# Kernel optimization log

Measured on AMD Instinct MI355X. Metric: run time of the kernel, lower is better.

## Reference

```python
import jax, jax.numpy as jnp
import numpy as np

B, L, D = 16, 2048, 320          # batch, frames, stacked feature dim (80 mel * 4 reduction)
CODEBOOK_SIZE, CODEBOOK_DIM = 8192, 16


def setup_inputs() -> dict:
    key = jax.random.key(0)
    k1, k2, k3 = jax.random.split(key, 3)
    masked_target_values = jax.random.normal(k1, (B, L, D), dtype=jnp.float32)
    # xavier_uniform_ for shape (D, codebook_dim): bound = sqrt(6/(fan_in+fan_out))
    bound = np.sqrt(6.0 / (D + CODEBOOK_DIM)).astype(np.float32)
    project_mat = jax.random.uniform(k2, (D, CODEBOOK_DIM), dtype=jnp.float32,
                                     minval=-bound, maxval=bound)
    cb = jax.random.normal(k3, (CODEBOOK_SIZE, CODEBOOK_DIM), dtype=jnp.float32)
    codebook_norm = cb / jnp.maximum(jnp.linalg.norm(cb, axis=-1, keepdims=True), 1e-12)
    return {"masked_target_values": masked_target_values,
            "project_mat": project_mat,
            "codebook_norm": codebook_norm}


def reference(masked_target_values, project_mat, codebook_norm):
    # project: (B, L, D) @ (D, K) -> (B, L, K)
    targets = jnp.einsum('bld,dk->blk', masked_target_values, project_mat)
    # L2 normalize along last dim (torch F.normalize with eps=1e-12)
    targets_norm = targets / jnp.maximum(
        jnp.linalg.norm(targets, axis=-1, keepdims=True), 1e-12)
    x2 = jnp.sum(targets_norm * targets_norm, axis=-1, keepdims=True)      # (B, L, 1)
    c2 = jnp.sum(codebook_norm * codebook_norm, axis=-1)                   # (C,)
    xc = jnp.einsum('blk,ck->blc', targets_norm, codebook_norm)            # (B, L, C)
    d2 = jnp.maximum(x2 + c2[None, None, :] - 2.0 * xc, 0.0)
    vector_distances = jnp.sqrt(d2)
    labels = jnp.argmin(vector_distances, axis=-1)                         # (B, L) int
    return labels
```

## Files before the change

kernel.cpp:

```cpp
#include <hip/hip_runtime.h>
#include <cfloat>

#define TOKENS 32768
#define DIM    320
#define NCODE  8192
#define PROW   20
#define APAD   40
#define NTILE  64
#define CERT_UNITS 32u

typedef __attribute__((ext_vector_type(8)))  short short8;
typedef __attribute__((ext_vector_type(16))) float f32x16;
typedef unsigned short ushort_t;
typedef unsigned int   uint_t;

static __device__ __forceinline__ ushort_t f2bf(float f) {
    uint_t u = __float_as_uint(f);
    u += 0x7fffu + ((u >> 16) & 1u);
    return (ushort_t)(u >> 16);
}
static __device__ __forceinline__ float bf2f(ushort_t h) {
    return __uint_as_float(((uint_t)h) << 16);
}
static __device__ __forceinline__ uint_t pack2(ushort_t a, ushort_t b) {
    return (uint_t)a | ((uint_t)b << 16);
}
static __device__ __forceinline__ uint_t umaxu(uint_t a, uint_t b) { return a > b ? a : b; }
static __device__ __forceinline__ uint_t uminu(uint_t a, uint_t b) { return a < b ? a : b; }

__global__ __launch_bounds__(256) void pack_kernel(
    const float* __restrict__ cb,
    float* __restrict__ c2o,
    ushort_t* __restrict__ cbpack)
{
    int j = blockIdx.x * 256 + threadIdx.x;
    const float4* cr4 = (const float4*)(cb + (size_t)j * 16);
    float4 c0 = cr4[0], c1 = cr4[1], c2v = cr4[2], c3 = cr4[3];
    float c[16] = {c0.x, c0.y, c0.z, c0.w, c1.x, c1.y, c1.z, c1.w,
                   c2v.x, c2v.y, c2v.z, c2v.w, c3.x, c3.y, c3.z, c3.w};
    float s = 0.f;
    #pragma unroll
    for (int k = 0; k < 16; ++k) s = fmaf(c[k], c[k], s);
    c2o[j] = s;
    ushort_t hi[16], lo[16];
    #pragma unroll
    for (int k = 0; k < 16; ++k) {
        hi[k] = f2bf(c[k]);
        lo[k] = f2bf(c[k] - bf2f(hi[k]));
    }
    uint4* dst = (uint4*)(cbpack + (size_t)j * 32);
    dst[0] = make_uint4(pack2(hi[0], hi[1]), pack2(hi[2], hi[3]),
                        pack2(hi[4], hi[5]), pack2(hi[6], hi[7]));
    dst[1] = make_uint4(pack2(hi[8], hi[9]), pack2(hi[10], hi[11]),
                        pack2(hi[12], hi[13]), pack2(hi[14], hi[15]));
    dst[2] = make_uint4(pack2(lo[0], lo[1]), pack2(lo[2], lo[3]),
                        pack2(lo[4], lo[5]), pack2(lo[6], lo[7]));
    dst[3] = make_uint4(pack2(lo[8], lo[9]), pack2(lo[10], lo[11]),
                        pack2(lo[12], lo[13]), pack2(lo[14], lo[15]));
}

__global__ __launch_bounds__(256, 2) void fused_kernel(
    const float* __restrict__ x,
    const float* __restrict__ P,
    const float* __restrict__ cb,
    const float* __restrict__ c2g,
    const ushort_t* __restrict__ cbpack,
    int* __restrict__ out)
{
    __shared__ float Ps[DIM * PROW];
    __shared__ ushort_t ApackS[32 * APAD];
    __shared__ float tnS[32 * 16];
    __shared__ float x2S[32];
    __shared__ uint_t mergeS[4][32][2];
    __shared__ int flagS[36];
    __shared__ float redE[4];
    __shared__ int   redI[4];

    int tid = threadIdx.x;
    if (tid == 0) flagS[32] = 0;

    {
        const float4* P4 = (const float4*)P;
        #pragma unroll
        for (int i = 0; i < 5; ++i) {
            int idx = tid + i * 256;
            int row = idx >> 2, col = idx & 3;
            *(float4*)(Ps + row * PROW + col * 4) = P4[idx];
        }
    }
    __syncthreads();

    int sub = tid & 7;
    int tk  = tid >> 3;
    int tok = blockIdx.x * 32 + tk;
    {
        const float* xr = x + (size_t)tok * DIM;
        float acc[16];
        #pragma unroll
        for (int k = 0; k < 16; ++k) acc[k] = 0.f;
        for (int i = 0; i < 40; ++i) {
            int d = i * 8 + sub;
            float xv = xr[d];
            const float4* pr = (const float4*)(Ps + d * PROW);
            float4 p0 = pr[0], p1 = pr[1], p2 = pr[2], p3 = pr[3];
            acc[0] = fmaf(xv, p0.x, acc[0]);   acc[1] = fmaf(xv, p0.y, acc[1]);
            acc[2] = fmaf(xv, p0.z, acc[2]);   acc[3] = fmaf(xv, p0.w, acc[3]);
            acc[4] = fmaf(xv, p1.x, acc[4]);   acc[5] = fmaf(xv, p1.y, acc[5]);
            acc[6] = fmaf(xv, p1.z, acc[6]);   acc[7] = fmaf(xv, p1.w, acc[7]);
            acc[8] = fmaf(xv, p2.x, acc[8]);   acc[9] = fmaf(xv, p2.y, acc[9]);
            acc[10] = fmaf(xv, p2.z, acc[10]); acc[11] = fmaf(xv, p2.w, acc[11]);
            acc[12] = fmaf(xv, p3.x, acc[12]); acc[13] = fmaf(xv, p3.y, acc[13]);
            acc[14] = fmaf(xv, p3.z, acc[14]); acc[15] = fmaf(xv, p3.w, acc[15]);
        }
        #pragma unroll
        for (int m = 1; m <= 4; m <<= 1) {
            #pragma unroll
            for (int k = 0; k < 16; ++k)
                acc[k] += __shfl_xor(acc[k], m);
        }
        float ss = 0.f;
        #pragma unroll
        for (int k = 0; k < 16; ++k) ss = fmaf(acc[k], acc[k], ss);
        float nrm = fmaxf(sqrtf(ss), 1e-12f);
        float inv = 1.0f / nrm;
        float t[16];
        #pragma unroll
        for (int k = 0; k < 16; ++k) t[k] = acc[k] * inv;
        float xx = 0.f;
        #pragma unroll
        for (int k = 0; k < 16; ++k) xx = fmaf(t[k], t[k], xx);

        ushort_t hi[16], lo[16];
        #pragma unroll
        for (int k = 0; k < 16; ++k) {
            hi[k] = f2bf(t[k]);
            lo[k] = f2bf(t[k] - bf2f(hi[k]));
        }
        if (sub < 4) {
            *(float4*)(tnS + tk * 16 + sub * 4) =
                make_float4(t[4 * sub], t[4 * sub + 1], t[4 * sub + 2], t[4 * sub + 3]);
        }
        uint4* dst = (uint4*)(ApackS + tk * APAD);
        if (sub == 4) dst[0] = make_uint4(pack2(hi[0], hi[1]), pack2(hi[2], hi[3]),
                                          pack2(hi[4], hi[5]), pack2(hi[6], hi[7]));
        if (sub == 5) dst[1] = make_uint4(pack2(hi[8], hi[9]), pack2(hi[10], hi[11]),
                                          pack2(hi[12], hi[13]), pack2(hi[14], hi[15]));
        if (sub == 6) dst[2] = make_uint4(pack2(lo[0], lo[1]), pack2(lo[2], lo[3]),
                                          pack2(lo[4], lo[5]), pack2(lo[6], lo[7]));
        if (sub == 7) dst[3] = make_uint4(pack2(lo[8], lo[9]), pack2(lo[10], lo[11]),
                                          pack2(lo[12], lo[13]), pack2(lo[14], lo[15]));
        if (sub == 0) x2S[tk] = xx;
    }
    __syncthreads();

    int lane = tid & 63;
    int wave = tid >> 6;
    int half = lane >> 5;
    int l31  = lane & 31;
    {
        short8 hiA = *(const short8*)(ApackS + l31 * APAD + half * 8);
        short8 loA = *(const short8*)(ApackS + l31 * APAD + 16 + half * 8);

        f32x16 zero = {};
        uint_t p1[16], p2[16];
        #pragma unroll
        for (int r = 0; r < 16; ++r) { p1[r] = 0u; p2[r] = 0u; }

        int base = wave * (NTILE * 32) + l31;

        const ushort_t* cp0 = cbpack + (size_t)base * 32;
        short8 hiB0 = *(const short8*)(cp0 + half * 8);
        short8 loB0 = *(const short8*)(cp0 + 16 + half * 8);
        f32x16 accP = __builtin_amdgcn_mfma_f32_32x32x16_bf16(hiA, hiB0, zero, 0, 0, 0);
        accP = __builtin_amdgcn_mfma_f32_32x32x16_bf16(loA, hiB0, accP, 0, 0, 0);
        accP = __builtin_amdgcn_mfma_f32_32x32x16_bf16(hiA, loB0, accP, 0, 0, 0);
        uint_t invP = 8191u - (uint_t)base;

        #pragma unroll 2
        for (int t = 1; t < NTILE; ++t) {
            int crow = base + t * 32;
            const ushort_t* cp = cbpack + (size_t)crow * 32;
            short8 hiB = *(const short8*)(cp + half * 8);
            short8 loB = *(const short8*)(cp + 16 + half * 8);

            #pragma unroll
            for (int r = 0; r < 16; ++r) {
                float kf = fmaf(accP[r], 131072.0f, 131072.0f);
                uint_t ku = (uint_t)kf;
                uint_t p  = (ku << 13) | invP;
                p2[r] = umaxu(p2[r], uminu(p, p1[r]));
                p1[r] = umaxu(p1[r], p);
            }

            f32x16 acc = __builtin_amdgcn_mfma_f32_32x32x16_bf16(hiA, hiB, zero, 0, 0, 0);
            acc = __builtin_amdgcn_mfma_f32_32x32x16_bf16(loA, hiB, acc, 0, 0, 0);
            acc = __builtin_amdgcn_mfma_f32_32x32x16_bf16(hiA, loB, acc, 0, 0, 0);
            accP = acc;
            invP = 8191u - (uint_t)crow;
        }
        #pragma unroll
        for (int r = 0; r < 16; ++r) {
            float kf = fmaf(accP[r], 131072.0f, 131072.0f);
            uint_t ku = (uint_t)kf;
            uint_t p  = (ku << 13) | invP;
            p2[r] = umaxu(p2[r], uminu(p, p1[r]));
            p1[r] = umaxu(p1[r], p);
        }

        #pragma unroll
        for (int mask = 1; mask <= 16; mask <<= 1) {
            #pragma unroll
            for (int r = 0; r < 16; ++r) {
                uint_t a1 = (uint_t)__shfl_xor((int)p1[r], mask);
                uint_t a2 = (uint_t)__shfl_xor((int)p2[r], mask);
                uint_t np2 = umaxu(uminu(p1[r], a1), umaxu(p2[r], a2));
                p1[r] = umaxu(p1[r], a1);
                p2[r] = np2;
            }
        }
        #pragma unroll
        for (int r = 0; r < 16; ++r) {
            if (l31 == r) {
                int mrow = (r & 3) + 8 * (r >> 2) + 4 * half;
                mergeS[wave][mrow][0] = p1[r];
                mergeS[wave][mrow][1] = p2[r];
            }
        }
    }
    __syncthreads();

    if (tid < 32) {
        uint_t p1 = mergeS[0][tid][0], p2 = mergeS[0][tid][1];
        #pragma unroll
        for (int w = 1; w < 4; ++w) {
            uint_t a1 = mergeS[w][tid][0];
            uint_t a2 = mergeS[w][tid][1];
            uint_t np2 = umaxu(uminu(p1, a1), umaxu(p2, a2));
            p1 = umaxu(p1, a1);
            p2 = np2;
        }
        if ((p1 >> 13) - (p2 >> 13) <= CERT_UNITS) {
            int pz = atomicAdd(&flagS[32], 1);
            flagS[pz] = tid;
        } else {
            out[blockIdx.x * 32 + tid] = 8191 - (int)(p1 & 8191u);
        }
    }
    __syncthreads();

    int nf = flagS[32];
    for (int fi = 0; fi < nf; ++fi) {
        int ftk = flagS[fi];
        float a[16];
        #pragma unroll
        for (int k = 0; k < 16; ++k) a[k] = tnS[ftk * 16 + k];
        float xx = x2S[ftk];
        float mn = FLT_MAX;
        int   id = 0x7fffffff;
        for (int c = 0; c < 32; ++c) {
            int j = c * 256 + tid;
            const float4* c4 = (const float4*)(cb + (size_t)j * 16);
            float4 c0 = c4[0], c1 = c4[1], c2v = c4[2], c3 = c4[3];
            float dot = 0.f;
            dot = fmaf(a[0], c0.x, dot);   dot = fmaf(a[1], c0.y, dot);
            dot = fmaf(a[2], c0.z, dot);   dot = fmaf(a[3], c0.w, dot);
            dot = fmaf(a[4], c1.x, dot);   dot = fmaf(a[5], c1.y, dot);
            dot = fmaf(a[6], c1.z, dot);   dot = fmaf(a[7], c1.w, dot);
            dot = fmaf(a[8], c2v.x, dot);  dot = fmaf(a[9], c2v.y, dot);
            dot = fmaf(a[10], c2v.z, dot); dot = fmaf(a[11], c2v.w, dot);
            dot = fmaf(a[12], c3.x, dot);  dot = fmaf(a[13], c3.y, dot);
            dot = fmaf(a[14], c3.z, dot);  dot = fmaf(a[15], c3.w, dot);
            float e = fmaf(-2.f, dot, xx + c2g[j]);
            if (e < mn || (e == mn && j < id)) { mn = e; id = j; }
        }
        #pragma unroll
        for (int mask = 1; mask <= 32; mask <<= 1) {
            float pmn = __shfl_xor(mn, mask);
            int   pid = __shfl_xor(id, mask);
            if (pmn < mn || (pmn == mn && pid < id)) { mn = pmn; id = pid; }
        }
        if (lane == 0) { redE[wave] = mn; redI[wave] = id; }
        __syncthreads();
        if (tid == 0) {
            #pragma unroll
            for (int w = 1; w < 4; ++w) {
                float pe = redE[w]; int pi = redI[w];
                if (pe < mn || (pe == mn && pi < id)) { mn = pe; id = pi; }
            }
            out[blockIdx.x * 32 + ftk] = id;
        }
        __syncthreads();
    }
}

extern "C" void kernel_launch(void* const* d_in, const int* in_sizes, int n_in,
                              void* d_out, int out_size, void* d_ws, size_t ws_size,
                              hipStream_t stream) {
    const float* x   = (const float*)d_in[0];
    const float* P   = (const float*)d_in[1];
    const float* cbn = (const float*)d_in[2];

    float*    c2     = (float*)d_ws;
    ushort_t* cbpack = (ushort_t*)(c2 + NCODE);
    int* labels = (int*)d_out;

    pack_kernel<<<NCODE / 256, 256, 0, stream>>>(cbn, c2, cbpack);
    fused_kernel<<<TOKENS / 32, 256, 0, stream>>>(x, P, cbn, c2, cbpack, labels);
}
```

Before: 170.5 us.

## Fold score scaling into A operand, use signed med3/max3 top-2 tracking

Pre-scales the normalized query by 2^17 before the bf16 hi/lo split, so the MFMA output can be converted to an integer directly without a per-element fma. Switches the packed score/index keys to signed ints and tracks top-2 across two codebook tiles at once using v_med3_i32 and v_max3_i32, halving the update steps per tile. The loop is unrolled to compute two tiles per iteration with loads issued ahead. The certification margin is nudged to cover the changed rounding, at the cost of slightly different fallback frequency and more register pressure from two accumulators.

```diff
diff --git a/kernel.cpp b/kernel.cpp
--- a/kernel.cpp
+++ b/kernel.cpp
@@ -7,7 +7,7 @@
 #define PROW   20
 #define APAD   40
 #define NTILE  64
-#define CERT_UNITS 32u
+#define CERT_UNITS 34
 
 typedef __attribute__((ext_vector_type(8)))  short short8;
 typedef __attribute__((ext_vector_type(16))) float f32x16;
@@ -25,8 +25,14 @@
 static __device__ __forceinline__ uint_t pack2(ushort_t a, ushort_t b) {
     return (uint_t)a | ((uint_t)b << 16);
 }
-static __device__ __forceinline__ uint_t umaxu(uint_t a, uint_t b) { return a > b ? a : b; }
-static __device__ __forceinline__ uint_t uminu(uint_t a, uint_t b) { return a < b ? a : b; }
+static __device__ __forceinline__ int imaxi(int a, int b) { return a > b ? a : b; }
+static __device__ __forceinline__ int imini(int a, int b) { return a < b ? a : b; }
+static __device__ __forceinline__ int med3i(int a, int b, int c) {
+    int d; asm("v_med3_i32 %0, %1, %2, %3" : "=v"(d) : "v"(a), "v"(b), "v"(c)); return d;
+}
+static __device__ __forceinline__ int max3i(int a, int b, int c) {
+    int d; asm("v_max3_i32 %0, %1, %2, %3" : "=v"(d) : "v"(a), "v"(b), "v"(c)); return d;
+}
 
 __global__ __launch_bounds__(256) void pack_kernel(
     const float* __restrict__ cb,
@@ -71,7 +77,7 @@
     __shared__ ushort_t ApackS[32 * APAD];
     __shared__ float tnS[32 * 16];
     __shared__ float x2S[32];
-    __shared__ uint_t mergeS[4][32][2];
+    __shared__ int mergeS[4][32][2];
     __shared__ int flagS[36];
     __shared__ float redE[4];
     __shared__ int   redI[4];
@@ -133,8 +139,9 @@
         ushort_t hi[16], lo[16];
         #pragma unroll
         for (int k = 0; k < 16; ++k) {
-            hi[k] = f2bf(t[k]);
-            lo[k] = f2bf(t[k] - bf2f(hi[k]));
+            float th = t[k] * 131072.0f;
+            hi[k] = f2bf(th);
+            lo[k] = f2bf(th - bf2f(hi[k]));
         }
         if (sub < 4) {
             *(float4*)(tnS + tk * 16 + sub * 4) =
@@ -162,59 +169,72 @@
         short8 loA = *(const short8*)(ApackS + l31 * APAD + 16 + half * 8);
 
         f32x16 zero = {};
-        uint_t p1[16], p2[16];
-        #pragma unroll
-        for (int r = 0; r < 16; ++r) { p1[r] = 0u; p2[r] = 0u; }
+        int p1[16], p2[16];
+        #pragma unroll
+        for (int r = 0; r < 16; ++r) { p1[r] = (int)0x80000000; p2[r] = (int)0x80000000; }
 
         int base = wave * (NTILE * 32) + l31;
-
-        const ushort_t* cp0 = cbpack + (size_t)base * 32;
-        short8 hiB0 = *(const short8*)(cp0 + half * 8);
-        short8 loB0 = *(const short8*)(cp0 + 16 + half * 8);
-        f32x16 accP = __builtin_amdgcn_mfma_f32_32x32x16_bf16(hiA, hiB0, zero, 0, 0, 0);
-        accP = __builtin_amdgcn_mfma_f32_32x32x16_bf16(loA, hiB0, accP, 0, 0, 0);
-        accP = __builtin_amdgcn_mfma_f32_32x32x16_bf16(hiA, loB0, accP, 0, 0, 0);
-        uint_t invP = 8191u - (uint_t)base;
+        const ushort_t* cpb = cbpack + (size_t)base * 32;
+
+        short8 hiB0 = *(const short8*)(cpb + half * 8);
+        short8 loB0 = *(const short8*)(cpb + 16 + half * 8);
+        short8 hiB1 = *(const short8*)(cpb + 1024 + half * 8);
+        short8 loB1 = *(const short8*)(cpb + 1024 + 16 + half * 8);
+        f32x16 accA = __builtin_amdgcn_mfma_f32_32x32x16_bf16(hiA, hiB0, zero, 0, 0, 0);
+        accA = __builtin_amdgcn_mfma_f32_32x32x16_bf16(loA, hiB0, accA, 0, 0, 0);
+        accA = __builtin_amdgcn_mfma_f32_32x32x16_bf16(hiA, loB0, accA, 0, 0, 0);
+        f32x16 accB = __builtin_amdgcn_mfma_f32_32x32x16_bf16(hiA, hiB1, zero, 0, 0, 0);
+        accB = __builtin_amdgcn_mfma_f32_32x32x16_bf16(loA, hiB1, accB, 0, 0, 0);
+        accB = __builtin_amdgcn_mfma_f32_32x32x16_bf16(hiA, loB1, accB, 0, 0, 0);
+        int invA = 8191 - base;
+        int invB = invA - 32;
 
         #pragma unroll 2
-        for (int t = 1; t < NTILE; ++t) {
-            int crow = base + t * 32;
-            const ushort_t* cp = cbpack + (size_t)crow * 32;
-            short8 hiB = *(const short8*)(cp + half * 8);
-            short8 loB = *(const short8*)(cp + 16 + half * 8);
+        for (int tp = 1; tp < NTILE / 2; ++tp) {
+            const ushort_t* cp = cpb + (size_t)tp * 2048;
+            short8 nhiB0 = *(const short8*)(cp + half * 8);
+            short8 nloB0 = *(const short8*)(cp + 16 + half * 8);
+            short8 nhiB1 = *(const short8*)(cp + 1024 + half * 8);
+            short8 nloB1 = *(const short8*)(cp + 1024 + 16 + half * 8);
 
             #pragma unroll
             for (int r = 0; r < 16; ++r) {
-                float kf = fmaf(accP[r], 131072.0f, 131072.0f);
-                uint_t ku = (uint_t)kf;
-                uint_t p  = (ku << 13) | invP;
-                p2[r] = umaxu(p2[r], uminu(p, p1[r]));
-                p1[r] = umaxu(p1[r], p);
+                int ka = (int)accA[r];
+                int kb = (int)accB[r];
+                int pa = (int)(((uint_t)ka << 13) | (uint_t)invA);
+                int pb = (int)(((uint_t)kb << 13) | (uint_t)invB);
+                int m3 = med3i(p1[r], pa, pb);
+                p1[r] = max3i(p1[r], pa, pb);
+                p2[r] = imaxi(p2[r], m3);
             }
-
-            f32x16 acc = __builtin_amdgcn_mfma_f32_32x32x16_bf16(hiA, hiB, zero, 0, 0, 0);
-            acc = __builtin_amdgcn_mfma_f32_32x32x16_bf16(loA, hiB, acc, 0, 0, 0);
-            acc = __builtin_amdgcn_mfma_f32_32x32x16_bf16(hiA, loB, acc, 0, 0, 0);
-            accP = acc;
-            invP = 8191u - (uint_t)crow;
+            invA -= 64; invB -= 64;
+
+            accA = __builtin_amdgcn_mfma_f32_32x32x16_bf16(hiA, nhiB0, zero, 0, 0, 0);
+            accA = __builtin_amdgcn_mfma_f32_32x32x16_bf16(loA, nhiB0, accA, 0, 0, 0);
+            accA = __builtin_amdgcn_mfma_f32_32x32x16_bf16(hiA, nloB0, accA, 0, 0, 0);
+            accB = __builtin_amdgcn_mfma_f32_32x32x16_bf16(hiA, nhiB1, zero, 0, 0, 0);
+            accB = __builtin_amdgcn_mfma_f32_32x32x16_bf16(loA, nhiB1, accB, 0, 0, 0);
+            accB = __builtin_amdgcn_mfma_f32_32x32x16_bf16(hiA, nloB1, accB, 0, 0, 0);
         }
         #pragma unroll
         for (int r = 0; r < 16; ++r) {
-            float kf = fmaf(accP[r], 131072.0f, 131072.0f);
-            uint_t ku = (uint_t)kf;
-            uint_t p  = (ku << 13) | invP;
-            p2[r] = umaxu(p2[r], uminu(p, p1[r]));
-            p1[r] = umaxu(p1[r], p);
+            int ka = (int)accA[r];
+            int kb = (int)accB[r];
+            int pa = (int)(((uint_t)ka << 13) | (uint_t)invA);
+            int pb = (int)(((uint_t)kb << 13) | (uint_t)invB);
+            int m3 = med3i(p1[r], pa, pb);
+            p1[r] = max3i(p1[r], pa, pb);
+            p2[r] = imaxi(p2[r], m3);
         }
 
         #pragma unroll
         for (int mask = 1; mask <= 16; mask <<= 1) {
             #pragma unroll
             for (int r = 0; r < 16; ++r) {
-                uint_t a1 = (uint_t)__shfl_xor((int)p1[r], mask);
-                uint_t a2 = (uint_t)__shfl_xor((int)p2[r], mask);
-                uint_t np2 = umaxu(uminu(p1[r], a1), umaxu(p2[r], a2));
-                p1[r] = umaxu(p1[r], a1);
+                int a1 = __shfl_xor(p1[r], mask);
+                int a2 = __shfl_xor(p2[r], mask);
+                int np2 = imaxi(imini(p1[r], a1), imaxi(p2[r], a2));
+                p1[r] = imaxi(p1[r], a1);
                 p2[r] = np2;
             }
         }
@@ -230,20 +250,20 @@
     __syncthreads();
 
     if (tid < 32) {
-        uint_t p1 = mergeS[0][tid][0], p2 = mergeS[0][tid][1];
+        int p1 = mergeS[0][tid][0], p2 = mergeS[0][tid][1];
         #pragma unroll
         for (int w = 1; w < 4; ++w) {
-            uint_t a1 = mergeS[w][tid][0];
-            uint_t a2 = mergeS[w][tid][1];
-            uint_t np2 = umaxu(uminu(p1, a1), umaxu(p2, a2));
-            p1 = umaxu(p1, a1);
+            int a1 = mergeS[w][tid][0];
+            int a2 = mergeS[w][tid][1];
+            int np2 = imaxi(imini(p1, a1), imaxi(p2, a2));
+            p1 = imaxi(p1, a1);
             p2 = np2;
         }
-        if ((p1 >> 13) - (p2 >> 13) <= CERT_UNITS) {
+        if (((p1 >> 13) - (p2 >> 13)) <= CERT_UNITS) {
             int pz = atomicAdd(&flagS[32], 1);
             flagS[pz] = tid;
         } else {
-            out[blockIdx.x * 32 + tid] = 8191 - (int)(p1 & 8191u);
+            out[blockIdx.x * 32 + tid] = 8191 - (p1 & 8191);
         }
     }
     __syncthreads();
```

After: 166.8 us. -2.2%, faster.
